# Kernel tuning notes

Hardware: AMD Instinct MI355X
Metric: run time of the kernel (lower is better)

Reference implementation:

```python
import jax, jax.numpy as jnp
import numpy as np

N_NODES = 50000
N_EDGES = 800000
D_FEAT = 64
N_CLASSES = 40


def setup_inputs() -> dict:
    key = jax.random.key(0)
    ks = jax.random.split(key, 8)
    x = jax.random.normal(ks[0], (N_NODES, D_FEAT), dtype=jnp.float32)
    edge_index = jax.random.randint(ks[1], (2, N_EDGES), 0, N_NODES, dtype=jnp.int64)
    # GCNConv weights (glorot-ish scale) and post-aggregation biases
    s1 = 1.0 / np.sqrt(D_FEAT)
    W1 = jax.random.normal(ks[2], (D_FEAT, D_FEAT), dtype=jnp.float32) * s1
    b1 = jnp.zeros((D_FEAT,), dtype=jnp.float32)
    W2 = jax.random.normal(ks[3], (D_FEAT, D_FEAT), dtype=jnp.float32) * s1
    b2 = jnp.zeros((D_FEAT,), dtype=jnp.float32)
    W3 = jax.random.normal(ks[4], (D_FEAT, N_CLASSES), dtype=jnp.float32) * s1
    b3 = jnp.zeros((N_CLASSES,), dtype=jnp.float32)
    return {"x": x, "edge_index": edge_index, "W1": W1, "b1": b1,
            "W2": W2, "b2": b2, "W3": W3, "b3": b3}


def _gcn_layer(x, src, dst, norm, W, b, n_nodes):
    # dense transform then normalized neighbor aggregation (PyG GCNConv)
    h = x @ W                                   # [N, out]
    msgs = h[src] * norm[:, None]               # gather over edges [E+N, out]
    agg = jax.ops.segment_sum(msgs, dst, num_segments=n_nodes)
    return agg + b


def reference(x, edge_index, W1, b1, W2, b2, W3, b3):
    n = x.shape[0]
    loops = jnp.arange(n, dtype=edge_index.dtype)
    src = jnp.concatenate([edge_index[0], loops])   # add self-loops
    dst = jnp.concatenate([edge_index[1], loops])
    # symmetric normalization: deg over targets incl. self-loops
    deg = jax.ops.segment_sum(jnp.ones_like(dst, dtype=x.dtype), dst, num_segments=n)
    dinv = jnp.where(deg > 0, jax.lax.rsqrt(deg), 0.0)
    norm = dinv[src] * dinv[dst]                    # [E+N]
    for W, b in ((W1, b1), (W2, b2), (W3, b3)):
        x = jax.nn.relu(_gcn_layer(x, src, dst, norm, W, b, n))
        # dropout treated as identity (deterministic eval reference)
    return jax.nn.log_softmax(x, axis=-1)
```

## Files before the change

### kernel.cpp

```cpp
#include <hip/hip_runtime.h>
#include <math.h>


#define DF 64
#define TB 256
#define NPART 8

__device__ __forceinline__ unsigned short f2bf(float f) {
    union { float f; unsigned u; } c; c.f = f;
    unsigned u = c.u;
    return (unsigned short)((u + 0x7fffu + ((u >> 16) & 1u)) >> 16);
}
__device__ __forceinline__ float bf2f(unsigned short h) {
    union { unsigned u; float f; } c; c.u = ((unsigned)h) << 16;
    return c.f;
}
__device__ __forceinline__ unsigned pk2bf(float lo, float hi) {
    return (unsigned)f2bf(lo) | ((unsigned)f2bf(hi) << 16);
}
__device__ __forceinline__ void acc_bf16x8(uint4 v, float* a) {
    a[0] += bf2f((unsigned short)(v.x & 0xffffu));
    a[1] += bf2f((unsigned short)(v.x >> 16));
    a[2] += bf2f((unsigned short)(v.y & 0xffffu));
    a[3] += bf2f((unsigned short)(v.y >> 16));
    a[4] += bf2f((unsigned short)(v.z & 0xffffu));
    a[5] += bf2f((unsigned short)(v.z >> 16));
    a[6] += bf2f((unsigned short)(v.w & 0xffffu));
    a[7] += bf2f((unsigned short)(v.w >> 16));
}
__device__ __forceinline__ void acc_bf16x4(uint2 v, float* a) {
    a[0] += bf2f((unsigned short)(v.x & 0xffffu));
    a[1] += bf2f((unsigned short)(v.x >> 16));
    a[2] += bf2f((unsigned short)(v.y & 0xffffu));
    a[3] += bf2f((unsigned short)(v.y >> 16));
}

__global__ void zero_int_kernel(int* __restrict__ p, int n) {
    int i = blockIdx.x * blockDim.x + threadIdx.x;
    if (i < n) p[i] = 0;
}

__global__ void count_deg_part_kernel(const int* __restrict__ dst, int* __restrict__ deg,
                                      int e, int psize) {
    const int p   = blockIdx.x & (NPART - 1);
    const int sl  = blockIdx.x / NPART;
    const int nsl = gridDim.x / NPART;
    const int lo = p * psize, hi = lo + psize;
    for (int i = sl * TB + threadIdx.x; i < e; i += nsl * TB) {
        int d = dst[i];
        if (d >= lo && d < hi) atomicAdd(&deg[d], 1);
    }
}

__global__ void scan_block_kernel(const int* __restrict__ deg, int* __restrict__ ex,
                                  int* __restrict__ bsum, float* __restrict__ dinv, int n) {
    __shared__ int s[TB];
    const int t = threadIdx.x;
    const int i = blockIdx.x * TB + t;
    int v = (i < n) ? deg[i] : 0;
    if (i < n) dinv[i] = rsqrtf((float)(v + 1));
    s[t] = v; __syncthreads();
#pragma unroll
    for (int o = 1; o < TB; o <<= 1) {
        int u = (t >= o) ? s[t - o] : 0;
        __syncthreads();
        s[t] += u;
        __syncthreads();
    }
    if (i < n) ex[i] = s[t] - v;
    if (t == TB - 1) bsum[blockIdx.x] = s[TB - 1];
}

__global__ void add_offsets_kernel(int* __restrict__ ex, const int* __restrict__ bsum,
                                   int* __restrict__ cursor, int n, int nb) {
    __shared__ int s[TB];
    const int t = threadIdx.x;
    int v = (t < nb) ? bsum[t] : 0;
    s[t] = v; __syncthreads();
#pragma unroll
    for (int o = 1; o < TB; o <<= 1) {
        int u = (t >= o) ? s[t - o] : 0;
        __syncthreads();
        s[t] += u;
        __syncthreads();
    }
    const int boff = (blockIdx.x > 0) ? s[blockIdx.x - 1] : 0;
    const int i = blockIdx.x * TB + t;
    if (i < n) {
        int r = ex[i] + boff;
        ex[i] = r;
        cursor[i] = r;
    }
}

__global__ void fill_csr_part_kernel(const int* __restrict__ src, const int* __restrict__ dst,
                                     int* __restrict__ cursor,
                                     unsigned short* __restrict__ cidx, int e, int psize) {
    const int p   = blockIdx.x & (NPART - 1);
    const int sl  = blockIdx.x / NPART;
    const int nsl = gridDim.x / NPART;
    const int lo = p * psize, hi = lo + psize;
    for (int i = sl * TB + threadIdx.x; i < e; i += nsl * TB) {
        int d = dst[i];
        if (d >= lo && d < hi) {
            int pos = atomicAdd(&cursor[d], 1);
            cidx[pos] = (unsigned short)src[i];
        }
    }
}

template <int NC, typename TIN>
__global__ __launch_bounds__(256) void gemm_kernel(const TIN* __restrict__ X,
                                                   const float* __restrict__ W,
                                                   const float* __restrict__ dinv,
                                                   unsigned short* __restrict__ G, int M) {
    __shared__ float Ws[64 * NC];
    __shared__ float Xs[16][65];
    const int tx = threadIdx.x;
    const int ty = threadIdx.y;
    const int tid = ty * 16 + tx;
    for (int i = tid; i < 16 * NC; i += 256)
        ((float4*)Ws)[i] = ((const float4*)W)[i];
    const int row0 = blockIdx.x * 16;
    {
        if (sizeof(TIN) == 4) {
            const float* Xf = (const float*)X;
            int r = tid / 16, c4 = tid % 16;
            float4 v = (row0 + r < M) ? ((const float4*)(Xf + (size_t)(row0 + r) * 64))[c4]
                                      : make_float4(0.f, 0.f, 0.f, 0.f);
            Xs[r][c4 * 4 + 0] = v.x; Xs[r][c4 * 4 + 1] = v.y;
            Xs[r][c4 * 4 + 2] = v.z; Xs[r][c4 * 4 + 3] = v.w;
        } else if (tid < 128) {
            const unsigned short* Xh = (const unsigned short*)X;
            int r = tid >> 3, s = tid & 7;
            uint4 v = (row0 + r < M)
                        ? *(const uint4*)(Xh + (size_t)(row0 + r) * 64 + s * 8)
                        : make_uint4(0, 0, 0, 0);
            Xs[r][s * 8 + 0] = bf2f((unsigned short)(v.x & 0xffffu));
            Xs[r][s * 8 + 1] = bf2f((unsigned short)(v.x >> 16));
            Xs[r][s * 8 + 2] = bf2f((unsigned short)(v.y & 0xffffu));
            Xs[r][s * 8 + 3] = bf2f((unsigned short)(v.y >> 16));
            Xs[r][s * 8 + 4] = bf2f((unsigned short)(v.z & 0xffffu));
            Xs[r][s * 8 + 5] = bf2f((unsigned short)(v.z >> 16));
            Xs[r][s * 8 + 6] = bf2f((unsigned short)(v.w & 0xffffu));
            Xs[r][s * 8 + 7] = bf2f((unsigned short)(v.w >> 16));
        }
    }
    __syncthreads();
    const int row = row0 + ty;
    const int c0 = tx * 4;
    if (row < M && c0 < NC) {
        float a0 = 0.f, a1 = 0.f, a2 = 0.f, a3 = 0.f;
#pragma unroll
        for (int k = 0; k < 64; ++k) {
            float xk = Xs[ty][k];
            float4 w = ((const float4*)(Ws + (size_t)k * NC))[tx];
            a0 += xk * w.x; a1 += xk * w.y; a2 += xk * w.z; a3 += xk * w.w;
        }
        float di = dinv[row];
        ushort4 o;
        o.x = f2bf(a0 * di); o.y = f2bf(a1 * di);
        o.z = f2bf(a2 * di); o.w = f2bf(a3 * di);
        *((ushort4*)(G + (size_t)row * NC + c0)) = o;
    }
}

__global__ void agg64_kernel(const unsigned short* __restrict__ G,
                             const int* __restrict__ rowptr, const int* __restrict__ deg,
                             const unsigned short* __restrict__ cidx,
                             const float* __restrict__ dinv, const float* __restrict__ b,
                             unsigned short* __restrict__ Y, int M) {
    const int lane = threadIdx.x & 63;
    const int node = blockIdx.x * 4 + (threadIdx.x >> 6);
    if (node >= M) return;
    const int grp = lane >> 3;
    const int sub = lane & 7;
    const int start = rowptr[node];
    const int cnt = deg[node];

    float a[8] = {0.f, 0.f, 0.f, 0.f, 0.f, 0.f, 0.f, 0.f};
    float c[8] = {0.f, 0.f, 0.f, 0.f, 0.f, 0.f, 0.f, 0.f};

    for (int base = 0; base < cnt; base += 64) {
        const int nthis = min(64, cnt - base);
        int myidx = (lane < nthis) ? (int)cidx[start + base + lane] : 0;
        int j = 0;
        for (; j + 16 <= nthis; j += 16) {
            int s0 = __shfl(myidx, j + grp, 64);
            int s1 = __shfl(myidx, j + 8 + grp, 64);
            uint4 v0 = *(const uint4*)(G + (size_t)s0 * 64 + sub * 8);
            uint4 v1 = *(const uint4*)(G + (size_t)s1 * 64 + sub * 8);
            acc_bf16x8(v0, a);
            acc_bf16x8(v1, c);
        }
        if (j + 8 <= nthis) {
            int s0 = __shfl(myidx, j + grp, 64);
            uint4 v0 = *(const uint4*)(G + (size_t)s0 * 64 + sub * 8);
            acc_bf16x8(v0, a);
            j += 8;
        }
        const int rem = nthis - j;
        if (grp < rem) {
            int s0 = __shfl(myidx, j + grp, 64);
            uint4 v0 = *(const uint4*)(G + (size_t)s0 * 64 + sub * 8);
            acc_bf16x8(v0, c);
        }
    }
#pragma unroll
    for (int k = 0; k < 8; ++k) a[k] += c[k];
#pragma unroll
    for (int k = 0; k < 8; ++k) {
        a[k] += __shfl_xor(a[k], 8, 64);
        a[k] += __shfl_xor(a[k], 16, 64);
        a[k] += __shfl_xor(a[k], 32, 64);
    }
    if (grp != 0) return;
    uint4 sv = *(const uint4*)(G + (size_t)node * 64 + sub * 8);
    float self[8];
    self[0] = bf2f((unsigned short)(sv.x & 0xffffu)); self[1] = bf2f((unsigned short)(sv.x >> 16));
    self[2] = bf2f((unsigned short)(sv.y & 0xffffu)); self[3] = bf2f((unsigned short)(sv.y >> 16));
    self[4] = bf2f((unsigned short)(sv.z & 0xffffu)); self[5] = bf2f((unsigned short)(sv.z >> 16));
    self[6] = bf2f((unsigned short)(sv.w & 0xffffu)); self[7] = bf2f((unsigned short)(sv.w >> 16));
    float4 b0 = *(const float4*)(b + sub * 8);
    float4 b1 = *(const float4*)(b + sub * 8 + 4);
    const float di = dinv[node];
    float v[8];
    v[0] = fmaxf((a[0] + self[0]) * di + b0.x, 0.f);
    v[1] = fmaxf((a[1] + self[1]) * di + b0.y, 0.f);
    v[2] = fmaxf((a[2] + self[2]) * di + b0.z, 0.f);
    v[3] = fmaxf((a[3] + self[3]) * di + b0.w, 0.f);
    v[4] = fmaxf((a[4] + self[4]) * di + b1.x, 0.f);
    v[5] = fmaxf((a[5] + self[5]) * di + b1.y, 0.f);
    v[6] = fmaxf((a[6] + self[6]) * di + b1.z, 0.f);
    v[7] = fmaxf((a[7] + self[7]) * di + b1.w, 0.f);
    uint4 o;
    o.x = pk2bf(v[0], v[1]); o.y = pk2bf(v[2], v[3]);
    o.z = pk2bf(v[4], v[5]); o.w = pk2bf(v[6], v[7]);
    *((uint4*)(Y + (size_t)node * 64 + sub * 8)) = o;
}

__global__ void agg40_lsm_kernel(const unsigned short* __restrict__ G,
                                 const int* __restrict__ rowptr, const int* __restrict__ deg,
                                 const unsigned short* __restrict__ cidx,
                                 const float* __restrict__ dinv, const float* __restrict__ b,
                                 float* __restrict__ Y, int M) {
    constexpr int NC = 40;
    constexpr int NQ = 10;
    const int lane = threadIdx.x & 63;
    const int node = blockIdx.x * 4 + (threadIdx.x >> 6);
    if (node >= M) return;
    const int grp = lane >> 4;
    const int sub = lane & 15;
    const bool act = (sub < NQ);
    const int start = rowptr[node];
    const int cnt = deg[node];

    float a[4] = {0.f, 0.f, 0.f, 0.f};
    float c[4] = {0.f, 0.f, 0.f, 0.f};

    for (int base = 0; base < cnt; base += 64) {
        const int nthis = min(64, cnt - base);
        int myidx = (lane < nthis) ? (int)cidx[start + base + lane] : 0;
        int j = 0;
        for (; j + 8 <= nthis; j += 8) {
            int s0 = __shfl(myidx, j + grp, 64);
            int s1 = __shfl(myidx, j + 4 + grp, 64);
            if (act) {
                uint2 v0 = *(const uint2*)(G + (size_t)s0 * NC + sub * 4);
                uint2 v1 = *(const uint2*)(G + (size_t)s1 * NC + sub * 4);
                acc_bf16x4(v0, a);
                acc_bf16x4(v1, c);
            }
        }
        if (j + 4 <= nthis) {
            int s0 = __shfl(myidx, j + grp, 64);
            if (act) {
                uint2 v0 = *(const uint2*)(G + (size_t)s0 * NC + sub * 4);
                acc_bf16x4(v0, a);
            }
            j += 4;
        }
        const int rem = nthis - j;
        if (grp < rem) {
            int s0 = __shfl(myidx, j + grp, 64);
            if (act) {
                uint2 v0 = *(const uint2*)(G + (size_t)s0 * NC + sub * 4);
                acc_bf16x4(v0, c);
            }
        }
    }
#pragma unroll
    for (int k = 0; k < 4; ++k) a[k] += c[k];
#pragma unroll
    for (int k = 0; k < 4; ++k) {
        a[k] += __shfl_xor(a[k], 16, 64);
        a[k] += __shfl_xor(a[k], 32, 64);
    }
    float v[4];
    {
        float self[4] = {0.f, 0.f, 0.f, 0.f};
        float4 bb = make_float4(0.f, 0.f, 0.f, 0.f);
        if (act) {
            uint2 sv = *(const uint2*)(G + (size_t)node * NC + sub * 4);
            self[0] = bf2f((unsigned short)(sv.x & 0xffffu));
            self[1] = bf2f((unsigned short)(sv.x >> 16));
            self[2] = bf2f((unsigned short)(sv.y & 0xffffu));
            self[3] = bf2f((unsigned short)(sv.y >> 16));
            bb = *(const float4*)(b + sub * 4);
        }
        const float di = dinv[node];
        v[0] = fmaxf((a[0] + self[0]) * di + bb.x, 0.f);
        v[1] = fmaxf((a[1] + self[1]) * di + bb.y, 0.f);
        v[2] = fmaxf((a[2] + self[2]) * di + bb.z, 0.f);
        v[3] = fmaxf((a[3] + self[3]) * di + bb.w, 0.f);
    }
    float m = act ? fmaxf(fmaxf(v[0], v[1]), fmaxf(v[2], v[3])) : -INFINITY;
#pragma unroll
    for (int o = 1; o < 16; o <<= 1) m = fmaxf(m, __shfl_xor(m, o, 64));
    float es = act ? (expf(v[0] - m) + expf(v[1] - m) + expf(v[2] - m) + expf(v[3] - m)) : 0.f;
#pragma unroll
    for (int o = 1; o < 16; o <<= 1) es += __shfl_xor(es, o, 64);
    const float ls = logf(es);
    if (act && grp == 0) {
        *((float4*)(Y + (size_t)node * NC + sub * 4)) =
            make_float4(v[0] - m - ls, v[1] - m - ls, v[2] - m - ls, v[3] - m - ls);
    }
}

extern "C" void kernel_launch(void* const* d_in, const int* in_sizes, int n_in,
                              void* d_out, int out_size, void* d_ws, size_t ws_size,
                              hipStream_t stream) {
    const float* x  = (const float*)d_in[0];
    const int*   ei = (const int*)d_in[1];
    const float* W1 = (const float*)d_in[2];
    const float* b1 = (const float*)d_in[3];
    const float* W2 = (const float*)d_in[4];
    const float* b2 = (const float*)d_in[5];
    const float* W3 = (const float*)d_in[6];
    const float* b3 = (const float*)d_in[7];
    float* out = (float*)d_out;

    const int M  = in_sizes[0] / DF;
    const int E  = in_sizes[1] / 2;
    (void)ws_size; (void)n_in; (void)out_size;

    const int* src = ei;
    const int* dst = ei + E;

    const size_t Ma = ((size_t)M + 63) & ~63ull;
    const size_t Ea = ((size_t)E + 63) & ~63ull;

    int* deg    = (int*)d_ws;
    int* rowptr = deg + Ma;
    int* cursor = rowptr + Ma;
    int* bsum   = cursor + Ma;
    unsigned short* cidx = (unsigned short*)(bsum + 256);
    float* dinv = (float*)(cidx + Ea);
    unsigned short* G    = (unsigned short*)(dinv + Ma);
    unsigned short* Bact = G + Ma * DF;

    const int gN = (M + TB - 1) / TB;
    const int nb = gN;
    const int psize = (M + NPART - 1) / NPART;
    const int partGrd = NPART * 96;

    zero_int_kernel<<<gN, TB, 0, stream>>>(deg, M);
    count_deg_part_kernel<<<partGrd, TB, 0, stream>>>(dst, deg, E, psize);
    scan_block_kernel<<<nb, TB, 0, stream>>>(deg, rowptr, bsum, dinv, M);
    add_offsets_kernel<<<nb, TB, 0, stream>>>(rowptr, bsum, cursor, M, nb);
    fill_csr_part_kernel<<<partGrd, TB, 0, stream>>>(src, dst, cursor, cidx, E, psize);

    const dim3 gemmBlk(16, 16);
    const int  gemmGrd = (M + 15) / 16;
    const int  aggGrd  = (M + 3) / 4;

    gemm_kernel<64, float><<<gemmGrd, gemmBlk, 0, stream>>>(x, W1, dinv, G, M);
    agg64_kernel<<<aggGrd, TB, 0, stream>>>(G, rowptr, deg, cidx, dinv, b1, Bact, M);
    gemm_kernel<64, unsigned short><<<gemmGrd, gemmBlk, 0, stream>>>(Bact, W2, dinv, G, M);
    agg64_kernel<<<aggGrd, TB, 0, stream>>>(G, rowptr, deg, cidx, dinv, b2, Bact, M);
    gemm_kernel<40, unsigned short><<<gemmGrd, gemmBlk, 0, stream>>>(Bact, W3, dinv, G, M);
    agg40_lsm_kernel<<<aggGrd, TB, 0, stream>>>(G, rowptr, deg, cidx, dinv, b3, out, M);
}
```

Baseline: 215.4 us.

## Fuse next layer's dense transform into the aggregation kernel epilogue

Layer-2 and layer-3 GEMMs are folded into the aggregation kernels: after computing the ReLU'd node row, each wavefront broadcasts the 64 values by shuffle and multiplies by the next weight matrix held in shared memory, writing the pre-scaled bf16 G for the next layer. This removes two gemm launches and the bf16 activation round trip through global memory. In exchange every aggregation block reloads W into LDS and adds a 64-step shuffle plus FMA epilogue per node, with only up to 64 or 40 lanes active.

```diff
diff --git a/kernel.cpp b/kernel.cpp
--- a/kernel.cpp
+++ b/kernel.cpp
@@ -14,9 +14,6 @@
 __device__ __forceinline__ float bf2f(unsigned short h) {
     union { unsigned u; float f; } c; c.u = ((unsigned)h) << 16;
     return c.f;
-}
-__device__ __forceinline__ unsigned pk2bf(float lo, float hi) {
-    return (unsigned)f2bf(lo) | ((unsigned)f2bf(hi) << 16);
 }
 __device__ __forceinline__ void acc_bf16x8(uint4 v, float* a) {
     a[0] += bf2f((unsigned short)(v.x & 0xffffu));
@@ -109,69 +106,59 @@
     }
 }
 
-template <int NC, typename TIN>
-__global__ __launch_bounds__(256) void gemm_kernel(const TIN* __restrict__ X,
+__global__ __launch_bounds__(256) void gemm_kernel(const float* __restrict__ X,
                                                    const float* __restrict__ W,
                                                    const float* __restrict__ dinv,
                                                    unsigned short* __restrict__ G, int M) {
-    __shared__ float Ws[64 * NC];
+    __shared__ float Ws[64 * 64];
     __shared__ float Xs[16][65];
     const int tx = threadIdx.x;
     const int ty = threadIdx.y;
     const int tid = ty * 16 + tx;
-    for (int i = tid; i < 16 * NC; i += 256)
+    for (int i = tid; i < 16 * 64; i += 256)
         ((float4*)Ws)[i] = ((const float4*)W)[i];
     const int row0 = blockIdx.x * 16;
     {
-        if (sizeof(TIN) == 4) {
-            const float* Xf = (const float*)X;
-            int r = tid / 16, c4 = tid % 16;
-            float4 v = (row0 + r < M) ? ((const float4*)(Xf + (size_t)(row0 + r) * 64))[c4]
-                                      : make_float4(0.f, 0.f, 0.f, 0.f);
-            Xs[r][c4 * 4 + 0] = v.x; Xs[r][c4 * 4 + 1] = v.y;
-            Xs[r][c4 * 4 + 2] = v.z; Xs[r][c4 * 4 + 3] = v.w;
-        } else if (tid < 128) {
-            const unsigned short* Xh = (const unsigned short*)X;
-            int r = tid >> 3, s = tid & 7;
-            uint4 v = (row0 + r < M)
-                        ? *(const uint4*)(Xh + (size_t)(row0 + r) * 64 + s * 8)
-                        : make_uint4(0, 0, 0, 0);
-            Xs[r][s * 8 + 0] = bf2f((unsigned short)(v.x & 0xffffu));
-            Xs[r][s * 8 + 1] = bf2f((unsigned short)(v.x >> 16));
-            Xs[r][s * 8 + 2] = bf2f((unsigned short)(v.y & 0xffffu));
-            Xs[r][s * 8 + 3] = bf2f((unsigned short)(v.y >> 16));
-            Xs[r][s * 8 + 4] = bf2f((unsigned short)(v.z & 0xffffu));
-            Xs[r][s * 8 + 5] = bf2f((unsigned short)(v.z >> 16));
-            Xs[r][s * 8 + 6] = bf2f((unsigned short)(v.w & 0xffffu));
-            Xs[r][s * 8 + 7] = bf2f((unsigned short)(v.w >> 16));
-        }
+        int r = tid / 16, c4 = tid % 16;
+        float4 v = (row0 + r < M) ? ((const float4*)(X + (size_t)(row0 + r) * 64))[c4]
+                                  : make_float4(0.f, 0.f, 0.f, 0.f);
+        Xs[r][c4 * 4 + 0] = v.x; Xs[r][c4 * 4 + 1] = v.y;
+        Xs[r][c4 * 4 + 2] = v.z; Xs[r][c4 * 4 + 3] = v.w;
     }
     __syncthreads();
     const int row = row0 + ty;
-    const int c0 = tx * 4;
-    if (row < M && c0 < NC) {
+    if (row < M) {
         float a0 = 0.f, a1 = 0.f, a2 = 0.f, a3 = 0.f;
 #pragma unroll
         for (int k = 0; k < 64; ++k) {
             float xk = Xs[ty][k];
-            float4 w = ((const float4*)(Ws + (size_t)k * NC))[tx];
+            float4 w = ((const float4*)(Ws + (size_t)k * 64))[tx];
             a0 += xk * w.x; a1 += xk * w.y; a2 += xk * w.z; a3 += xk * w.w;
         }
         float di = dinv[row];
         ushort4 o;
         o.x = f2bf(a0 * di); o.y = f2bf(a1 * di);
         o.z = f2bf(a2 * di); o.w = f2bf(a3 * di);
-        *((ushort4*)(G + (size_t)row * NC + c0)) = o;
-    }
-}
-
-__global__ void agg64_kernel(const unsigned short* __restrict__ G,
-                             const int* __restrict__ rowptr, const int* __restrict__ deg,
-                             const unsigned short* __restrict__ cidx,
-                             const float* __restrict__ dinv, const float* __restrict__ b,
-                             unsigned short* __restrict__ Y, int M) {
-    const int lane = threadIdx.x & 63;
-    const int node = blockIdx.x * 4 + (threadIdx.x >> 6);
+        *((ushort4*)(G + (size_t)row * 64 + tx * 4)) = o;
+    }
+}
+
+template <int NCO>
+__global__ __launch_bounds__(256) void aggemv_kernel(
+        const unsigned short* __restrict__ G,
+        const int* __restrict__ rowptr, const int* __restrict__ deg,
+        const unsigned short* __restrict__ cidx,
+        const float* __restrict__ dinv, const float* __restrict__ b,
+        const float* __restrict__ Wn,
+        unsigned short* __restrict__ Gout, int M) {
+    __shared__ float Ws[64 * NCO];
+    const int tid = threadIdx.x;
+    for (int i = tid; i < 16 * NCO; i += 256)
+        ((float4*)Ws)[i] = ((const float4*)Wn)[i];
+    __syncthreads();
+
+    const int lane = tid & 63;
+    const int node = blockIdx.x * 4 + (tid >> 6);
     if (node >= M) return;
     const int grp = lane >> 3;
     const int sub = lane & 7;
@@ -214,29 +201,35 @@
         a[k] += __shfl_xor(a[k], 16, 64);
         a[k] += __shfl_xor(a[k], 32, 64);
     }
-    if (grp != 0) return;
     uint4 sv = *(const uint4*)(G + (size_t)node * 64 + sub * 8);
-    float self[8];
-    self[0] = bf2f((unsigned short)(sv.x & 0xffffu)); self[1] = bf2f((unsigned short)(sv.x >> 16));
-    self[2] = bf2f((unsigned short)(sv.y & 0xffffu)); self[3] = bf2f((unsigned short)(sv.y >> 16));
-    self[4] = bf2f((unsigned short)(sv.z & 0xffffu)); self[5] = bf2f((unsigned short)(sv.z >> 16));
-    self[6] = bf2f((unsigned short)(sv.w & 0xffffu)); self[7] = bf2f((unsigned short)(sv.w >> 16));
     float4 b0 = *(const float4*)(b + sub * 8);
     float4 b1 = *(const float4*)(b + sub * 8 + 4);
     const float di = dinv[node];
     float v[8];
-    v[0] = fmaxf((a[0] + self[0]) * di + b0.x, 0.f);
-    v[1] = fmaxf((a[1] + self[1]) * di + b0.y, 0.f);
-    v[2] = fmaxf((a[2] + self[2]) * di + b0.z, 0.f);
-    v[3] = fmaxf((a[3] + self[3]) * di + b0.w, 0.f);
-    v[4] = fmaxf((a[4] + self[4]) * di + b1.x, 0.f);
-    v[5] = fmaxf((a[5] + self[5]) * di + b1.y, 0.f);
-    v[6] = fmaxf((a[6] + self[6]) * di + b1.z, 0.f);
-    v[7] = fmaxf((a[7] + self[7]) * di + b1.w, 0.f);
-    uint4 o;
-    o.x = pk2bf(v[0], v[1]); o.y = pk2bf(v[2], v[3]);
-    o.z = pk2bf(v[4], v[5]); o.w = pk2bf(v[6], v[7]);
-    *((uint4*)(Y + (size_t)node * 64 + sub * 8)) = o;
+    v[0] = fmaxf((a[0] + bf2f((unsigned short)(sv.x & 0xffffu))) * di + b0.x, 0.f);
+    v[1] = fmaxf((a[1] + bf2f((unsigned short)(sv.x >> 16)))     * di + b0.y, 0.f);
+    v[2] = fmaxf((a[2] + bf2f((unsigned short)(sv.y & 0xffffu))) * di + b0.z, 0.f);
+    v[3] = fmaxf((a[3] + bf2f((unsigned short)(sv.y >> 16)))     * di + b0.w, 0.f);
+    v[4] = fmaxf((a[4] + bf2f((unsigned short)(sv.z & 0xffffu))) * di + b1.x, 0.f);
+    v[5] = fmaxf((a[5] + bf2f((unsigned short)(sv.z >> 16)))     * di + b1.y, 0.f);
+    v[6] = fmaxf((a[6] + bf2f((unsigned short)(sv.w & 0xffffu))) * di + b1.z, 0.f);
+    v[7] = fmaxf((a[7] + bf2f((unsigned short)(sv.w >> 16)))     * di + b1.w, 0.f);
+
+    float acc0 = 0.f, acc1 = 0.f;
+#pragma unroll
+    for (int s = 0; s < 8; s += 2) {
+#pragma unroll
+        for (int j = 0; j < 8; ++j) {
+            float y0 = __shfl(v[j], s, 64);
+            float y1 = __shfl(v[j], s + 1, 64);
+            if (lane < NCO) {
+                acc0 += y0 * Ws[(s * 8 + j) * NCO + lane];
+                acc1 += y1 * Ws[((s + 1) * 8 + j) * NCO + lane];
+            }
+        }
+    }
+    if (lane < NCO)
+        Gout[(size_t)node * NCO + lane] = f2bf((acc0 + acc1) * di);
 }
 
 __global__ void agg40_lsm_kernel(const unsigned short* __restrict__ G,
@@ -356,8 +349,8 @@
     int* bsum   = cursor + Ma;
     unsigned short* cidx = (unsigned short*)(bsum + 256);
     float* dinv = (float*)(cidx + Ea);
-    unsigned short* G    = (unsigned short*)(dinv + Ma);
-    unsigned short* Bact = G + Ma * DF;
+    unsigned short* G0 = (unsigned short*)(dinv + Ma);
+    unsigned short* G1 = G0 + Ma * DF;
 
     const int gN = (M + TB - 1) / TB;
     const int nb = gN;
@@ -374,10 +367,8 @@
     const int  gemmGrd = (M + 15) / 16;
     const int  aggGrd  = (M + 3) / 4;
 
-    gemm_kernel<64, float><<<gemmGrd, gemmBlk, 0, stream>>>(x, W1, dinv, G, M);
-    agg64_kernel<<<aggGrd, TB, 0, stream>>>(G, rowptr, deg, cidx, dinv, b1, Bact, M);
-    gemm_kernel<64, unsigned short><<<gemmGrd, gemmBlk, 0, stream>>>(Bact, W2, dinv, G, M);
-    agg64_kernel<<<aggGrd, TB, 0, stream>>>(G, rowptr, deg, cidx, dinv, b2, Bact, M);
-    gemm_kernel<40, unsigned short><<<gemmGrd, gemmBlk, 0, stream>>>(Bact, W3, dinv, G, M);
-    agg40_lsm_kernel<<<aggGrd, TB, 0, stream>>>(G, rowptr, deg, cidx, dinv, b3, out, M);
-}
+    gemm_kernel<<<gemmGrd, gemmBlk, 0, stream>>>(x, W1, dinv, G0, M);
+    aggemv_kernel<64><<<aggGrd, TB, 0, stream>>>(G0, rowptr, deg, cidx, dinv, b1, W2, G1, M);
+    aggemv_kernel<40><<<aggGrd, TB, 0, stream>>>(G1, rowptr, deg, cidx, dinv, b2, W3, G0, M);
+    agg40_lsm_kernel<<<aggGrd, TB, 0, stream>>>(G0, rowptr, deg, cidx, dinv, b3, out, M);
+}
```

Result: slower. 264.6 us (+22.8%).

## Replace FP32 shared-memory GEMM with bf16 MFMA per-wave 16-row tiles

Applied to the files above, without the earlier changes.

The dense transform kernel is replaced by a matrix-core version in which each wavefront computes a 16-row tile using two mfma_f32_16x16x32_bf16 instructions per 16-column tile. Weights are loaded from global memory and converted to bf16 in registers by every wave, so shared memory and block barriers are no longer used. The first layer's input and the weights are now rounded to bf16 before multiplying, which lowers precision. Output stores become scalar 16-bit writes spread over rows instead of vectorised row stores.

```diff
diff --git a/kernel.cpp b/kernel.cpp
--- a/kernel.cpp
+++ b/kernel.cpp
@@ -5,6 +5,9 @@
 #define DF 64
 #define TB 256
 #define NPART 8
+
+typedef __attribute__((ext_vector_type(8))) short bf16x8;
+typedef __attribute__((ext_vector_type(4))) float f32x4;
 
 __device__ __forceinline__ unsigned short f2bf(float f) {
     union { float f; unsigned u; } c; c.f = f;
@@ -14,9 +17,6 @@
 __device__ __forceinline__ float bf2f(unsigned short h) {
     union { unsigned u; float f; } c; c.u = ((unsigned)h) << 16;
     return c.f;
-}
-__device__ __forceinline__ unsigned pk2bf(float lo, float hi) {
-    return (unsigned)f2bf(lo) | ((unsigned)f2bf(hi) << 16);
 }
 __device__ __forceinline__ void acc_bf16x8(uint4 v, float* a) {
     a[0] += bf2f((unsigned short)(v.x & 0xffffu));
@@ -109,59 +109,75 @@
     }
 }
 
-template <int NC, typename TIN>
-__global__ __launch_bounds__(256) void gemm_kernel(const TIN* __restrict__ X,
-                                                   const float* __restrict__ W,
-                                                   const float* __restrict__ dinv,
-                                                   unsigned short* __restrict__ G, int M) {
-    __shared__ float Ws[64 * NC];
-    __shared__ float Xs[16][65];
-    const int tx = threadIdx.x;
-    const int ty = threadIdx.y;
-    const int tid = ty * 16 + tx;
-    for (int i = tid; i < 16 * NC; i += 256)
-        ((float4*)Ws)[i] = ((const float4*)W)[i];
-    const int row0 = blockIdx.x * 16;
-    {
-        if (sizeof(TIN) == 4) {
-            const float* Xf = (const float*)X;
-            int r = tid / 16, c4 = tid % 16;
-            float4 v = (row0 + r < M) ? ((const float4*)(Xf + (size_t)(row0 + r) * 64))[c4]
-                                      : make_float4(0.f, 0.f, 0.f, 0.f);
-            Xs[r][c4 * 4 + 0] = v.x; Xs[r][c4 * 4 + 1] = v.y;
-            Xs[r][c4 * 4 + 2] = v.z; Xs[r][c4 * 4 + 3] = v.w;
-        } else if (tid < 128) {
-            const unsigned short* Xh = (const unsigned short*)X;
-            int r = tid >> 3, s = tid & 7;
-            uint4 v = (row0 + r < M)
-                        ? *(const uint4*)(Xh + (size_t)(row0 + r) * 64 + s * 8)
-                        : make_uint4(0, 0, 0, 0);
-            Xs[r][s * 8 + 0] = bf2f((unsigned short)(v.x & 0xffffu));
-            Xs[r][s * 8 + 1] = bf2f((unsigned short)(v.x >> 16));
-            Xs[r][s * 8 + 2] = bf2f((unsigned short)(v.y & 0xffffu));
-            Xs[r][s * 8 + 3] = bf2f((unsigned short)(v.y >> 16));
-            Xs[r][s * 8 + 4] = bf2f((unsigned short)(v.z & 0xffffu));
-            Xs[r][s * 8 + 5] = bf2f((unsigned short)(v.z >> 16));
-            Xs[r][s * 8 + 6] = bf2f((unsigned short)(v.w & 0xffffu));
-            Xs[r][s * 8 + 7] = bf2f((unsigned short)(v.w >> 16));
-        }
-    }
-    __syncthreads();
-    const int row = row0 + ty;
-    const int c0 = tx * 4;
-    if (row < M && c0 < NC) {
-        float a0 = 0.f, a1 = 0.f, a2 = 0.f, a3 = 0.f;
-#pragma unroll
-        for (int k = 0; k < 64; ++k) {
-            float xk = Xs[ty][k];
-            float4 w = ((const float4*)(Ws + (size_t)k * NC))[tx];
-            a0 += xk * w.x; a1 += xk * w.y; a2 += xk * w.z; a3 += xk * w.w;
-        }
-        float di = dinv[row];
-        ushort4 o;
-        o.x = f2bf(a0 * di); o.y = f2bf(a1 * di);
-        o.z = f2bf(a2 * di); o.w = f2bf(a3 * di);
-        *((ushort4*)(G + (size_t)row * NC + c0)) = o;
+template <int NCO, typename TIN>
+__global__ __launch_bounds__(256) void gemm_mfma_kernel(
+        const TIN* __restrict__ X, const float* __restrict__ W,
+        const float* __restrict__ dinv, unsigned short* __restrict__ G, int M) {
+    constexpr int NCT = (NCO + 15) / 16;
+    const int lane = threadIdx.x & 63;
+    const int wid  = threadIdx.x >> 6;
+    const int t    = blockIdx.x * 4 + wid;
+    const int nt   = (M + 15) >> 4;
+    if (t >= nt) return;
+    const int n = lane & 15;
+    const int g = lane >> 4;
+
+    bf16x8 bf[NCT][2];
+#pragma unroll
+    for (int ct = 0; ct < NCT; ++ct) {
+        const int c = ct * 16 + n;
+#pragma unroll
+        for (int ks = 0; ks < 2; ++ks) {
+#pragma unroll
+            for (int j = 0; j < 8; ++j) {
+                const int k = ks * 32 + g * 8 + j;
+                float w = (c < NCO) ? W[k * NCO + c] : 0.f;
+                bf[ct][ks][j] = (short)f2bf(w);
+            }
+        }
+    }
+
+    const int row_a = t * 16 + n;
+    const int ra = (row_a < M) ? row_a : (M - 1);
+    bf16x8 af[2];
+    if (sizeof(TIN) == 4) {
+        const float* Xf = (const float*)X;
+#pragma unroll
+        for (int ks = 0; ks < 2; ++ks) {
+            float4 p0 = *(const float4*)(Xf + (size_t)ra * 64 + ks * 32 + g * 8);
+            float4 p1 = *(const float4*)(Xf + (size_t)ra * 64 + ks * 32 + g * 8 + 4);
+            af[ks][0] = (short)f2bf(p0.x); af[ks][1] = (short)f2bf(p0.y);
+            af[ks][2] = (short)f2bf(p0.z); af[ks][3] = (short)f2bf(p0.w);
+            af[ks][4] = (short)f2bf(p1.x); af[ks][5] = (short)f2bf(p1.y);
+            af[ks][6] = (short)f2bf(p1.z); af[ks][7] = (short)f2bf(p1.w);
+        }
+    } else {
+        const short* Xh = (const short*)X;
+#pragma unroll
+        for (int ks = 0; ks < 2; ++ks)
+            af[ks] = *(const bf16x8*)(Xh + (size_t)ra * 64 + ks * 32 + g * 8);
+    }
+
+    const int rbase = t * 16 + g * 4;
+    float di[4];
+#pragma unroll
+    for (int r = 0; r < 4; ++r) {
+        int rr = rbase + r;
+        di[r] = dinv[(rr < M) ? rr : (M - 1)];
+    }
+
+#pragma unroll
+    for (int ct = 0; ct < NCT; ++ct) {
+        f32x4 acc = {0.f, 0.f, 0.f, 0.f};
+        acc = __builtin_amdgcn_mfma_f32_16x16x32_bf16(af[0], bf[ct][0], acc, 0, 0, 0);
+        acc = __builtin_amdgcn_mfma_f32_16x16x32_bf16(af[1], bf[ct][1], acc, 0, 0, 0);
+        const int col = ct * 16 + n;
+#pragma unroll
+        for (int r = 0; r < 4; ++r) {
+            const int row = rbase + r;
+            if (row < M && col < NCO)
+                G[(size_t)row * NCO + col] = f2bf(acc[r] * di[r]);
+        }
     }
 }
 
@@ -234,8 +250,10 @@
     v[6] = fmaxf((a[6] + self[6]) * di + b1.z, 0.f);
     v[7] = fmaxf((a[7] + self[7]) * di + b1.w, 0.f);
     uint4 o;
-    o.x = pk2bf(v[0], v[1]); o.y = pk2bf(v[2], v[3]);
-    o.z = pk2bf(v[4], v[5]); o.w = pk2bf(v[6], v[7]);
+    o.x = (unsigned)f2bf(v[0]) | ((unsigned)f2bf(v[1]) << 16);
+    o.y = (unsigned)f2bf(v[2]) | ((unsigned)f2bf(v[3]) << 16);
+    o.z = (unsigned)f2bf(v[4]) | ((unsigned)f2bf(v[5]) << 16);
+    o.w = (unsigned)f2bf(v[6]) | ((unsigned)f2bf(v[7]) << 16);
     *((uint4*)(Y + (size_t)node * 64 + sub * 8)) = o;
 }
 
@@ -356,8 +374,8 @@
     int* bsum   = cursor + Ma;
     unsigned short* cidx = (unsigned short*)(bsum + 256);
     float* dinv = (float*)(cidx + Ea);
-    unsigned short* G    = (unsigned short*)(dinv + Ma);
-    unsigned short* Bact = G + Ma * DF;
+    unsigned short* G0 = (unsigned short*)(dinv + Ma);
+    unsigned short* G1 = G0 + Ma * DF;
 
     const int gN = (M + TB - 1) / TB;
     const int nb = gN;
@@ -370,14 +388,14 @@
     add_offsets_kernel<<<nb, TB, 0, stream>>>(rowptr, bsum, cursor, M, nb);
     fill_csr_part_kernel<<<partGrd, TB, 0, stream>>>(src, dst, cursor, cidx, E, psize);
 
-    const dim3 gemmBlk(16, 16);
-    const int  gemmGrd = (M + 15) / 16;
-    const int  aggGrd  = (M + 3) / 4;
-
-    gemm_kernel<64, float><<<gemmGrd, gemmBlk, 0, stream>>>(x, W1, dinv, G, M);
-    agg64_kernel<<<aggGrd, TB, 0, stream>>>(G, rowptr, deg, cidx, dinv, b1, Bact, M);
-    gemm_kernel<64, unsigned short><<<gemmGrd, gemmBlk, 0, stream>>>(Bact, W2, dinv, G, M);
-    agg64_kernel<<<aggGrd, TB, 0, stream>>>(G, rowptr, deg, cidx, dinv, b2, Bact, M);
-    gemm_kernel<40, unsigned short><<<gemmGrd, gemmBlk, 0, stream>>>(Bact, W3, dinv, G, M);
-    agg40_lsm_kernel<<<aggGrd, TB, 0, stream>>>(G, rowptr, deg, cidx, dinv, b3, out, M);
-}
+    const int nt      = (M + 15) / 16;
+    const int gemmGrd = (nt + 3) / 4;
+    const int aggGrd  = (M + 3) / 4;
+
+    gemm_mfma_kernel<64, float><<<gemmGrd, TB, 0, stream>>>(x, W1, dinv, G0, M);
+    agg64_kernel<<<aggGrd, TB, 0, stream>>>(G0, rowptr, deg, cidx, dinv, b1, G1, M);
+    gemm_mfma_kernel<64, unsigned short><<<gemmGrd, TB, 0, stream>>>(G1, W2, dinv, G0, M);
+    agg64_kernel<<<aggGrd, TB, 0, stream>>>(G0, rowptr, deg, cidx, dinv, b2, G1, M);
+    gemm_mfma_kernel<40, unsigned short><<<gemmGrd, TB, 0, stream>>>(G1, W3, dinv, G0, M);
+    agg40_lsm_kernel<<<aggGrd, TB, 0, stream>>>(G0, rowptr, deg, cidx, dinv, b3, out, M);
+}
```

After: 196.4 us. 1.1x faster.
